# Optimization experiments

Measured on AMD Instinct MI355X. Metric: run time of the kernel, lower is better.

## Reference

```python
import jax, jax.numpy as jnp
import numpy as np

NUM_HEADS = 16

def setup_inputs() -> dict:
    key = jax.random.key(0)
    kq, kk, kv = jax.random.split(key, 3)
    B, S, D = 4, 2048, 1024
    return {
        "queries": jax.random.normal(kq, (B, S, D), dtype=jnp.float32),
        "keys": jax.random.normal(kk, (B, S, D), dtype=jnp.float32),
        "values": jax.random.normal(kv, (B, S, D), dtype=jnp.float32),
    }

def _split_heads(x):
    # [B, S, D] -> [B, H, S, Dh]
    B, S, D = x.shape
    return x.reshape(B, S, NUM_HEADS, D // NUM_HEADS).transpose(0, 2, 1, 3)

def reference(queries, keys, values):
    q = _split_heads(queries)   # [B, H, S, Dh]
    k = _split_heads(keys)
    v = _split_heads(values)
    d_k = k.shape[-1]
    scale = 1.0 / jnp.sqrt(jnp.asarray(d_k, dtype=q.dtype))
    # [B, H, S, S] score matrix (materialized, as in the original bmm path)
    scores = jnp.einsum('bhqd,bhkd->bhqk', q, k) * scale
    weights = jax.nn.softmax(scores, axis=-1)
    out = jnp.einsum('bhqk,bhkd->bhqd', weights, v)  # [B, H, S, Dh]
    B, H, S, Dh = out.shape
    return out.transpose(0, 2, 1, 3).reshape(B, S, H * Dh)
```

## Files before the change

kernel.cpp:

```cpp
#include <hip/hip_runtime.h>
#include <hip/hip_bf16.h>
#include <math.h>

#define SEQ    2048
#define NH     16
#define DH     64
#define DMODEL 1024
#define KT     64
#define NT     (SEQ/KT)
#define KH_BYTES (4 * NH * SEQ * DH * 2)

typedef __bf16 bf16x8 __attribute__((ext_vector_type(8)));
typedef float  f32x4  __attribute__((ext_vector_type(4)));
typedef float  f32x16 __attribute__((ext_vector_type(16)));
typedef unsigned u32x2 __attribute__((ext_vector_type(2)));
typedef unsigned short u16x8 __attribute__((ext_vector_type(8)));
typedef __attribute__((address_space(3))) unsigned int        lds_u32_t;
typedef __attribute__((address_space(1))) const unsigned int  g_u32_t;

__device__ __forceinline__ ushort f2bf(float f) {
    union { __hip_bfloat16 h; ushort u; } z;
    z.h = __float2bfloat16(f);
    return z.u;
}

__device__ __forceinline__ unsigned pk2(float lo, float hi) {
    unsigned r;
    asm("v_cvt_pk_bf16_f32 %0, %1, %2" : "=v"(r) : "v"(lo), "v"(hi));
    return r;
}

__device__ __forceinline__ void load16(const char* g, char* l) {
    __builtin_amdgcn_global_load_lds((g_u32_t*)g, (lds_u32_t*)l, 16, 0, 0);
}

__global__ __launch_bounds__(256)
void prep_kv(const float* __restrict__ K, const float* __restrict__ V,
             ushort* __restrict__ Kh, ushort* __restrict__ Vt) {
    int blk = blockIdx.x;
    int tid = threadIdx.x;
    if (blk < 2048) {
        int i = tid >> 6;
        int c = tid & 63;
        int g = blk * 4 + i;
        int b = g >> 11, s = g & 2047;
        int h = c >> 2, d0 = (c & 3) * 16;
        const float* kp = K + (size_t)g * DMODEL + c * 16;
        float4 f0 = ((const float4*)kp)[0];
        float4 f1 = ((const float4*)kp)[1];
        float4 f2 = ((const float4*)kp)[2];
        float4 f3 = ((const float4*)kp)[3];
        u16x8 a, bq;
        a[0]=f2bf(f0.x); a[1]=f2bf(f0.y); a[2]=f2bf(f0.z); a[3]=f2bf(f0.w);
        a[4]=f2bf(f1.x); a[5]=f2bf(f1.y); a[6]=f2bf(f1.z); a[7]=f2bf(f1.w);
        bq[0]=f2bf(f2.x); bq[1]=f2bf(f2.y); bq[2]=f2bf(f2.z); bq[3]=f2bf(f2.w);
        bq[4]=f2bf(f3.x); bq[5]=f2bf(f3.y); bq[6]=f2bf(f3.z); bq[7]=f2bf(f3.w);
        ushort* op = Kh + ((size_t)(b * NH + h) * SEQ + s) * DH + d0;
        *(u16x8*)op = a;
        *(u16x8*)(op + 8) = bq;
    } else {
        int vb = blk - 2048;
        int st = vb & 31, bh = vb >> 5;
        int b = bh >> 4, h = bh & 15;
        int s0 = st * 64;
        int s4 = tid >> 4, dg = tid & 15;
        const float* vp = V + ((size_t)(b * SEQ + s0 + s4 * 4)) * DMODEL + h * DH + dg * 4;
        float4 r0 = ((const float4*)vp)[0];
        float4 r1 = *(const float4*)(vp + DMODEL);
        float4 r2 = *(const float4*)(vp + 2 * DMODEL);
        float4 r3 = *(const float4*)(vp + 3 * DMODEL);
        ushort4 w0 = make_ushort4(f2bf(r0.x), f2bf(r1.x), f2bf(r2.x), f2bf(r3.x));
        ushort4 w1 = make_ushort4(f2bf(r0.y), f2bf(r1.y), f2bf(r2.y), f2bf(r3.y));
        ushort4 w2 = make_ushort4(f2bf(r0.z), f2bf(r1.z), f2bf(r2.z), f2bf(r3.z));
        ushort4 w3 = make_ushort4(f2bf(r0.w), f2bf(r1.w), f2bf(r2.w), f2bf(r3.w));
        size_t vbase = ((size_t)bh * DH) * SEQ + s0 + s4 * 4;
        *(ushort4*)(Vt + vbase + (size_t)(dg * 4 + 0) * SEQ) = w0;
        *(ushort4*)(Vt + vbase + (size_t)(dg * 4 + 1) * SEQ) = w1;
        *(ushort4*)(Vt + vbase + (size_t)(dg * 4 + 2) * SEQ) = w2;
        *(ushort4*)(Vt + vbase + (size_t)(dg * 4 + 3) * SEQ) = w3;
    }
}

__global__ __launch_bounds__(256, 2)
void mha_fwd32(const float* __restrict__ Q, const ushort* __restrict__ Kh,
               const ushort* __restrict__ Vt, float* __restrict__ Out) {
    int raw = blockIdx.x;
    int bid = (raw & 7) * 64 + (raw >> 3);
    int qt = bid & 7;
    int bh = bid >> 3;
    int b = bh >> 4, h = bh & 15;

    const int tid  = threadIdx.x;
    const int lane = tid & 63;
    const int w    = tid >> 6;
    const int l31  = lane & 31;
    const int lh   = lane >> 5;

    __shared__ __attribute__((aligned(16))) ushort Ks[2][KT * DH];
    __shared__ __attribute__((aligned(16))) ushort Vs[2][KT * DH];

    int o0  = tid * 16;
    int o1  = o0 + 4096;
    int so0 = o0 ^ (((o0 >> 7) & 7) << 4);
    int so1 = o1 ^ (((o1 >> 7) & 7) << 4);
    const char* khead = (const char*)Kh + (size_t)bh * (SEQ * DH * 2);
    const char* vhead = (const char*)Vt + (size_t)bh * (SEQ * DH * 2);
    const char* kg0 = khead + so0;
    const char* kg1 = khead + so1;
    const char* vg0 = vhead + (size_t)(o0 >> 7) * (SEQ * 2) + (so0 & 127);
    const char* vg1 = vhead + (size_t)(o1 >> 7) * (SEQ * 2) + (so1 & 127);

    const float QSCALE = 0.125f * 1.4426950408889634f;
    bf16x8 qf[2][4];
    #pragma unroll
    for (int q2 = 0; q2 < 2; ++q2) {
        int qrow = qt * 256 + w * 64 + q2 * 32 + l31;
        const float* qp = Q + ((size_t)b * SEQ + qrow) * DMODEL + h * DH + lh * 8;
        #pragma unroll
        for (int ks = 0; ks < 4; ++ks) {
            float4 fa = *(const float4*)(qp + ks * 16);
            float4 fb = *(const float4*)(qp + ks * 16 + 4);
            union { unsigned u[4]; bf16x8 v; } z;
            z.u[0] = pk2(fa.x * QSCALE, fa.y * QSCALE);
            z.u[1] = pk2(fa.z * QSCALE, fa.w * QSCALE);
            z.u[2] = pk2(fb.x * QSCALE, fb.y * QSCALE);
            z.u[3] = pk2(fb.z * QSCALE, fb.w * QSCALE);
            qf[q2][ks] = z.v;
        }
    }

    f32x16 oacc[2][2];
    #pragma unroll
    for (int a = 0; a < 2; ++a)
        #pragma unroll
        for (int d = 0; d < 2; ++d)
            #pragma unroll
            for (int i = 0; i < 16; ++i) oacc[a][d][i] = 0.f;
    float lacc0 = 0.f, lacc1 = 0.f;

    int swz = (l31 & 7) << 4;
    int offRd[2][4];
    #pragma unroll
    for (int x = 0; x < 2; ++x)
        #pragma unroll
        for (int ks = 0; ks < 4; ++ks)
            offRd[x][ks] = (x * 32 + l31) * 128 + ((ks * 32 + lh * 16) ^ swz);

    {
        char* kb = (char*)&Ks[0][0] + w * 1024;
        char* vb = (char*)&Vs[0][0] + w * 1024;
        load16(kg0, kb); load16(kg1, kb + 4096);
        load16(vg0, vb); load16(vg1, vb + 4096);
        kg0 += KT * DH * 2; kg1 += KT * DH * 2; vg0 += KT * 2; vg1 += KT * 2;
    }
    __syncthreads();

    int buf = 0;
    for (int kt = 0; kt < NT; ++kt) {
        if (kt + 1 < NT) {
            char* kb = (char*)&Ks[buf ^ 1][0] + w * 1024;
            char* vb = (char*)&Vs[buf ^ 1][0] + w * 1024;
            load16(kg0, kb); load16(kg1, kb + 4096);
            load16(vg0, vb); load16(vg1, vb + 4096);
            kg0 += KT * DH * 2; kg1 += KT * DH * 2; vg0 += KT * 2; vg1 += KT * 2;
        }
        const char* kbb = (const char*)&Ks[buf][0];
        const char* vbb = (const char*)&Vs[buf][0];

        f32x16 sc[2][2];
        #pragma unroll
        for (int a = 0; a < 2; ++a)
            #pragma unroll
            for (int t = 0; t < 2; ++t)
                #pragma unroll
                for (int i = 0; i < 16; ++i) sc[a][t][i] = 0.f;

        __builtin_amdgcn_s_setprio(1);
        #pragma unroll
        for (int t = 0; t < 2; ++t) {
            #pragma unroll
            for (int ks = 0; ks < 4; ++ks) {
                bf16x8 kf = *(const bf16x8*)(kbb + offRd[t][ks]);
                sc[0][t] = __builtin_amdgcn_mfma_f32_32x32x16_bf16(kf, qf[0][ks], sc[0][t], 0, 0, 0);
                sc[1][t] = __builtin_amdgcn_mfma_f32_32x32x16_bf16(kf, qf[1][ks], sc[1][t], 0, 0, 0);
            }
        }
        __builtin_amdgcn_s_setprio(0);

        bf16x8 pa[2][4];
        #pragma unroll
        for (int q2 = 0; q2 < 2; ++q2) {
            float e[2][16];
            #pragma unroll
            for (int t = 0; t < 2; ++t)
                #pragma unroll
                for (int r = 0; r < 16; ++r)
                    e[t][r] = exp2f(fminf(sc[q2][t][r], 80.f));
            float s0 = 0.f, s1 = 0.f, s2 = 0.f, s3 = 0.f;
            #pragma unroll
            for (int t = 0; t < 2; ++t)
                #pragma unroll
                for (int m = 0; m < 4; ++m) {
                    s0 += e[t][4 * m + 0]; s1 += e[t][4 * m + 1];
                    s2 += e[t][4 * m + 2]; s3 += e[t][4 * m + 3];
                }
            if (q2 == 0) lacc0 += (s0 + s1) + (s2 + s3);
            else         lacc1 += (s0 + s1) + (s2 + s3);
            #pragma unroll
            for (int t = 0; t < 2; ++t) {
                #pragma unroll
                for (int s = 0; s < 2; ++s) {
                    unsigned X  = pk2(e[t][8 * s + 0], e[t][8 * s + 1]);
                    unsigned Bw = pk2(e[t][8 * s + 2], e[t][8 * s + 3]);
                    unsigned Y  = pk2(e[t][8 * s + 4], e[t][8 * s + 5]);
                    unsigned Dw = pk2(e[t][8 * s + 6], e[t][8 * s + 7]);
                    u32x2 pq = __builtin_amdgcn_permlane32_swap(X, Y, false, false);
                    u32x2 rs = __builtin_amdgcn_permlane32_swap(Bw, Dw, false, false);
                    union { unsigned u[4]; bf16x8 v; } z;
                    z.u[0] = pq.x; z.u[1] = rs.x; z.u[2] = pq.y; z.u[3] = rs.y;
                    pa[q2][2 * t + s] = z.v;
                }
            }
        }

        __builtin_amdgcn_s_setprio(1);
        #pragma unroll
        for (int dt = 0; dt < 2; ++dt) {
            #pragma unroll
            for (int ks = 0; ks < 4; ++ks) {
                bf16x8 vf = *(const bf16x8*)(vbb + offRd[dt][ks]);
                oacc[0][dt] = __builtin_amdgcn_mfma_f32_32x32x16_bf16(pa[0][ks], vf, oacc[0][dt], 0, 0, 0);
                oacc[1][dt] = __builtin_amdgcn_mfma_f32_32x32x16_bf16(pa[1][ks], vf, oacc[1][dt], 0, 0, 0);
            }
        }
        __builtin_amdgcn_s_setprio(0);

        __syncthreads();
        buf ^= 1;
    }

    #pragma unroll
    for (int q2 = 0; q2 < 2; ++q2) {
        float la = (q2 == 0) ? lacc0 : lacc1;
        float lt = la + __shfl_xor(la, 32);
        float rl = 1.0f / lt;
        #pragma unroll
        for (int r = 0; r < 16; ++r) {
            int qp_ = (r & 3) + 8 * (r >> 2) + 4 * lh;
            float rlr = __shfl(rl, (lane & 32) | qp_);
            int qrow = qt * 256 + w * 64 + q2 * 32 + qp_;
            float* op = Out + ((size_t)b * SEQ + qrow) * DMODEL + h * DH + l31;
            op[0]  = oacc[q2][0][r] * rlr;
            op[32] = oacc[q2][1][r] * rlr;
        }
    }
}

__global__ __launch_bounds__(256)
void mha_fwd_fallback(const float* __restrict__ Q, const float* __restrict__ K,
                      const float* __restrict__ V, float* __restrict__ Out) {
    int raw = blockIdx.x;
    int bid = (raw & 7) * 256 + (raw >> 3);
    int qt = bid & 31;
    int bh = bid >> 5;
    int b  = bh >> 4;
    int h  = bh & 15;
    const int tid  = threadIdx.x;
    const int lane = tid & 63;
    const int w    = tid >> 6;
    const int l15  = lane & 15;
    const int g    = lane >> 4;
    __shared__ ushort KsS[KT * DH];
    __shared__ ushort VTS[DH * KT];
    __shared__ ushort PlS[4][16 * KT];
    char* KsB = (char*)KsS;
    char* VTB = (char*)VTS;
    char* PlB = (char*)&PlS[w][0];
    const size_t base = ((size_t)b * SEQ) * DMODEL + (size_t)h * DH;
    const float QSCALE = 0.125f * 1.4426950408889634f;
    bf16x8 qa[2];
    {
        int qrow = qt * 64 + w * 16 + l15;
        const float* qp = Q + base + (size_t)qrow * DMODEL;
        for (int ds = 0; ds < 2; ++ds) {
            float4 f0 = *(const float4*)(qp + ds * 32 + g * 8);
            float4 f1 = *(const float4*)(qp + ds * 32 + g * 8 + 4);
            union { ushort u[8]; bf16x8 v; } pk;
            pk.u[0] = f2bf(f0.x * QSCALE); pk.u[1] = f2bf(f0.y * QSCALE);
            pk.u[2] = f2bf(f0.z * QSCALE); pk.u[3] = f2bf(f0.w * QSCALE);
            pk.u[4] = f2bf(f1.x * QSCALE); pk.u[5] = f2bf(f1.y * QSCALE);
            pk.u[6] = f2bf(f1.z * QSCALE); pk.u[7] = f2bf(f1.w * QSCALE);
            qa[ds] = pk.v;
        }
    }
    f32x4 oacc[4];
    for (int i = 0; i < 4; ++i) { oacc[i][0]=0.f; oacc[i][1]=0.f; oacc[i][2]=0.f; oacc[i][3]=0.f; }
    float m_r[4], l_r[4];
    for (int r = 0; r < 4; ++r) { m_r[r] = -3.0e38f; l_r[r] = 0.f; }
    for (int kt = 0; kt < SEQ / KT; ++kt) {
        const int kbase = kt * KT;
        for (int i = 0; i < 4; ++i) {
            int pos  = i * 256 + tid;
            int krow = pos >> 4;
            int d4   = (pos & 15) * 4;
            const float* kp = K + base + (size_t)(kbase + krow) * DMODEL + d4;
            float4 f = *(const float4*)kp;
            ushort4 u = make_ushort4(f2bf(f.x), f2bf(f.y), f2bf(f.z), f2bf(f.w));
            int off = (krow * 128 + d4 * 2) ^ ((krow & 7) << 4);
            *(ushort4*)(KsB + off) = u;
        }
        {
            int kg = tid >> 4;
            int d4 = (tid & 15) * 4;
            const float* vp = V + base + (size_t)(kbase + kg * 4) * DMODEL + d4;
            float4 r0 = *(const float4*)(vp);
            float4 r1 = *(const float4*)(vp + DMODEL);
            float4 r2 = *(const float4*)(vp + 2 * DMODEL);
            float4 r3 = *(const float4*)(vp + 3 * DMODEL);
            ushort4 c0 = make_ushort4(f2bf(r0.x), f2bf(r1.x), f2bf(r2.x), f2bf(r3.x));
            ushort4 c1 = make_ushort4(f2bf(r0.y), f2bf(r1.y), f2bf(r2.y), f2bf(r3.y));
            ushort4 c2 = make_ushort4(f2bf(r0.z), f2bf(r1.z), f2bf(r2.z), f2bf(r3.z));
            ushort4 c3 = make_ushort4(f2bf(r0.w), f2bf(r1.w), f2bf(r2.w), f2bf(r3.w));
            int row, off;
            row = d4 + 0; off = (row * 128 + kg * 8) ^ ((row & 7) << 4); *(ushort4*)(VTB + off) = c0;
            row = d4 + 1; off = (row * 128 + kg * 8) ^ ((row & 7) << 4); *(ushort4*)(VTB + off) = c1;
            row = d4 + 2; off = (row * 128 + kg * 8) ^ ((row & 7) << 4); *(ushort4*)(VTB + off) = c2;
            row = d4 + 3; off = (row * 128 + kg * 8) ^ ((row & 7) << 4); *(ushort4*)(VTB + off) = c3;
        }
        __syncthreads();
        f32x4 sc[4];
        for (int sub = 0; sub < 4; ++sub) {
            f32x4 a; a[0]=0.f; a[1]=0.f; a[2]=0.f; a[3]=0.f;
            for (int ds = 0; ds < 2; ++ds) {
                int krow = sub * 16 + l15;
                int off = (krow * 128 + ds * 64 + g * 16) ^ ((krow & 7) << 4);
                bf16x8 kb = *(const bf16x8*)(KsB + off);
                a = __builtin_amdgcn_mfma_f32_16x16x32_bf16(qa[ds], kb, a, 0, 0, 0);
            }
            sc[sub] = a;
        }
        float corr[4];
        float p[4][4];
        for (int r = 0; r < 4; ++r) {
            float t = fmaxf(fmaxf(sc[0][r], sc[1][r]), fmaxf(sc[2][r], sc[3][r]));
            t = fmaxf(t, __shfl_xor(t, 1));
            t = fmaxf(t, __shfl_xor(t, 2));
            t = fmaxf(t, __shfl_xor(t, 4));
            t = fmaxf(t, __shfl_xor(t, 8));
            float mn = fmaxf(m_r[r], t);
            corr[r] = exp2f(m_r[r] - mn);
            m_r[r] = mn;
            float s = 0.f;
            for (int sub = 0; sub < 4; ++sub) {
                float e = exp2f(sc[sub][r] - mn);
                p[sub][r] = e;
                s += e;
            }
            s += __shfl_xor(s, 1);
            s += __shfl_xor(s, 2);
            s += __shfl_xor(s, 4);
            s += __shfl_xor(s, 8);
            l_r[r] = l_r[r] * corr[r] + s;
        }
        for (int dsub = 0; dsub < 4; ++dsub)
            for (int r = 0; r < 4; ++r)
                oacc[dsub][r] *= corr[r];
        for (int r = 0; r < 4; ++r) {
            int row = g * 4 + r;
            for (int sub = 0; sub < 4; ++sub) {
                int off = (row * 128 + (sub * 16 + l15) * 2) ^ ((row & 7) << 4);
                *(ushort*)(PlB + off) = f2bf(p[sub][r]);
            }
        }
        bf16x8 pa[2];
        for (int ks = 0; ks < 2; ++ks) {
            int off = (l15 * 128 + ks * 64 + g * 16) ^ ((l15 & 7) << 4);
            pa[ks] = *(const bf16x8*)(PlB + off);
        }
        for (int dsub = 0; dsub < 4; ++dsub) {
            f32x4 a = oacc[dsub];
            for (int ks = 0; ks < 2; ++ks) {
                int row = dsub * 16 + l15;
                int off = (row * 128 + ks * 64 + g * 16) ^ ((row & 7) << 4);
                bf16x8 vb = *(const bf16x8*)(VTB + off);
                a = __builtin_amdgcn_mfma_f32_16x16x32_bf16(pa[ks], vb, a, 0, 0, 0);
            }
            oacc[dsub] = a;
        }
        __syncthreads();
    }
    for (int r = 0; r < 4; ++r) {
        float rl = 1.0f / l_r[r];
        int qrow = qt * 64 + w * 16 + g * 4 + r;
        float* op = Out + ((size_t)b * SEQ + qrow) * DMODEL + (size_t)h * DH;
        for (int dsub = 0; dsub < 4; ++dsub)
            op[dsub * 16 + l15] = oacc[dsub][r] * rl;
    }
}

extern "C" void kernel_launch(void* const* d_in, const int* in_sizes, int n_in,
                              void* d_out, int out_size, void* d_ws, size_t ws_size,
                              hipStream_t stream) {
    const float* Q = (const float*)d_in[0];
    const float* K = (const float*)d_in[1];
    const float* V = (const float*)d_in[2];
    float* Out = (float*)d_out;

    if (ws_size >= (size_t)2 * KH_BYTES) {
        ushort* Kh = (ushort*)d_ws;
        ushort* Vt = (ushort*)((char*)d_ws + KH_BYTES);
        prep_kv<<<dim3(4096), dim3(256), 0, stream>>>(K, V, Kh, Vt);
        mha_fwd32<<<dim3(512), dim3(256), 0, stream>>>(Q, Kh, Vt, Out);
    } else {
        mha_fwd_fallback<<<dim3(2048), dim3(256), 0, stream>>>(Q, K, V, Out);
    }
}
```

Baseline: 243.9 us.

## Compute softmax row sums via MFMA with ones and transpose V through LDS

The softmax denominator now comes from extra MFMAs that multiply the bf16 probabilities by a ones matrix, replacing the per-element VALU adds and the cross-lane shuffles. exp2f with clamping becomes the raw v_exp_f32 builtin, the first QK MFMA takes a zero accumulator instead of zero-initialising the score registers, and the final division uses the fast reciprocal. The V transpose in the prep kernel is staged through swizzled LDS so global reads and writes are coalesced. In exchange this adds 8 MFMAs per tile, computes the row sum from bf16-rounded probabilities, and drops the overflow clamp, which could affect accuracy.

```diff
diff --git a/kernel.cpp b/kernel.cpp
--- a/kernel.cpp
+++ b/kernel.cpp
@@ -30,6 +30,14 @@
     return r;
 }
 
+__device__ __forceinline__ float fexp2(float x) {
+#if __has_builtin(__builtin_amdgcn_exp2f)
+    return __builtin_amdgcn_exp2f(x);
+#else
+    float r; asm("v_exp_f32 %0, %1\n\ts_nop 0" : "=v"(r) : "v"(x)); return r;
+#endif
+}
+
 __device__ __forceinline__ void load16(const char* g, char* l) {
     __builtin_amdgcn_global_load_lds((g_u32_t*)g, (lds_u32_t*)l, 16, 0, 0);
 }
@@ -37,6 +45,7 @@
 __global__ __launch_bounds__(256)
 void prep_kv(const float* __restrict__ K, const float* __restrict__ V,
              ushort* __restrict__ Kh, ushort* __restrict__ Vt) {
+    __shared__ __attribute__((aligned(16))) ushort T[64 * 64];
     int blk = blockIdx.x;
     int tid = threadIdx.x;
     if (blk < 2048) {
@@ -63,21 +72,42 @@
         int st = vb & 31, bh = vb >> 5;
         int b = bh >> 4, h = bh & 15;
         int s0 = st * 64;
-        int s4 = tid >> 4, dg = tid & 15;
-        const float* vp = V + ((size_t)(b * SEQ + s0 + s4 * 4)) * DMODEL + h * DH + dg * 4;
-        float4 r0 = ((const float4*)vp)[0];
-        float4 r1 = *(const float4*)(vp + DMODEL);
-        float4 r2 = *(const float4*)(vp + 2 * DMODEL);
-        float4 r3 = *(const float4*)(vp + 3 * DMODEL);
-        ushort4 w0 = make_ushort4(f2bf(r0.x), f2bf(r1.x), f2bf(r2.x), f2bf(r3.x));
-        ushort4 w1 = make_ushort4(f2bf(r0.y), f2bf(r1.y), f2bf(r2.y), f2bf(r3.y));
-        ushort4 w2 = make_ushort4(f2bf(r0.z), f2bf(r1.z), f2bf(r2.z), f2bf(r3.z));
-        ushort4 w3 = make_ushort4(f2bf(r0.w), f2bf(r1.w), f2bf(r2.w), f2bf(r3.w));
-        size_t vbase = ((size_t)bh * DH) * SEQ + s0 + s4 * 4;
-        *(ushort4*)(Vt + vbase + (size_t)(dg * 4 + 0) * SEQ) = w0;
-        *(ushort4*)(Vt + vbase + (size_t)(dg * 4 + 1) * SEQ) = w1;
-        *(ushort4*)(Vt + vbase + (size_t)(dg * 4 + 2) * SEQ) = w2;
-        *(ushort4*)(Vt + vbase + (size_t)(dg * 4 + 3) * SEQ) = w3;
+        char* TB = (char*)T;
+        {
+            int sr = tid >> 2, seg = tid & 3;
+            const float* vp = V + ((size_t)(b * SEQ + s0 + sr)) * DMODEL + h * DH + seg * 16;
+            float4 f0 = ((const float4*)vp)[0];
+            float4 f1 = ((const float4*)vp)[1];
+            float4 f2 = ((const float4*)vp)[2];
+            float4 f3 = ((const float4*)vp)[3];
+            union { unsigned u[4]; u16x8 v; } za, zb;
+            za.u[0] = pk2(f0.x, f0.y); za.u[1] = pk2(f0.z, f0.w);
+            za.u[2] = pk2(f1.x, f1.y); za.u[3] = pk2(f1.z, f1.w);
+            zb.u[0] = pk2(f2.x, f2.y); zb.u[1] = pk2(f2.z, f2.w);
+            zb.u[2] = pk2(f3.x, f3.y); zb.u[3] = pk2(f3.z, f3.w);
+            int base = sr * 128 + seg * 32;
+            int sw = (sr & 7) << 4;
+            *(u16x8*)(TB + ((base) ^ sw))      = za.v;
+            *(u16x8*)(TB + ((base + 16) ^ sw)) = zb.v;
+        }
+        __syncthreads();
+        {
+            int dr = tid >> 2, sseg = tid & 3;
+            u16x8 o0, o1;
+            #pragma unroll
+            for (int i = 0; i < 8; ++i) {
+                int s = sseg * 16 + i;
+                o0[i] = *(const ushort*)(TB + ((s * 128 + dr * 2) ^ ((s & 7) << 4)));
+            }
+            #pragma unroll
+            for (int i = 0; i < 8; ++i) {
+                int s = sseg * 16 + 8 + i;
+                o1[i] = *(const ushort*)(TB + ((s * 128 + dr * 2) ^ ((s & 7) << 4)));
+            }
+            ushort* op = Vt + ((size_t)(bh * DH + dr)) * SEQ + s0 + sseg * 16;
+            *(u16x8*)op = o0;
+            *(u16x8*)(op + 8) = o1;
+        }
     }
 }
 
@@ -129,6 +159,17 @@
         }
     }
 
+    f32x16 zro;
+    #pragma unroll
+    for (int i = 0; i < 16; ++i) zro[i] = 0.f;
+    bf16x8 onesf;
+    {
+        union { unsigned u[4]; bf16x8 v; } z;
+        z.u[0] = 0x3F803F80u; z.u[1] = 0x3F803F80u;
+        z.u[2] = 0x3F803F80u; z.u[3] = 0x3F803F80u;
+        onesf = z.v;
+    }
+
     f32x16 oacc[2][2];
     #pragma unroll
     for (int a = 0; a < 2; ++a)
@@ -136,7 +177,11 @@
         for (int d = 0; d < 2; ++d)
             #pragma unroll
             for (int i = 0; i < 16; ++i) oacc[a][d][i] = 0.f;
-    float lacc0 = 0.f, lacc1 = 0.f;
+    f32x16 lacc[2];
+    #pragma unroll
+    for (int a = 0; a < 2; ++a)
+        #pragma unroll
+        for (int i = 0; i < 16; ++i) lacc[a][i] = 0.f;
 
     int swz = (l31 & 7) << 4;
     int offRd[2][4];
@@ -168,21 +213,19 @@
         const char* vbb = (const char*)&Vs[buf][0];
 
         f32x16 sc[2][2];
-        #pragma unroll
-        for (int a = 0; a < 2; ++a)
-            #pragma unroll
-            for (int t = 0; t < 2; ++t)
-                #pragma unroll
-                for (int i = 0; i < 16; ++i) sc[a][t][i] = 0.f;
-
         __builtin_amdgcn_s_setprio(1);
         #pragma unroll
         for (int t = 0; t < 2; ++t) {
             #pragma unroll
             for (int ks = 0; ks < 4; ++ks) {
                 bf16x8 kf = *(const bf16x8*)(kbb + offRd[t][ks]);
-                sc[0][t] = __builtin_amdgcn_mfma_f32_32x32x16_bf16(kf, qf[0][ks], sc[0][t], 0, 0, 0);
-                sc[1][t] = __builtin_amdgcn_mfma_f32_32x32x16_bf16(kf, qf[1][ks], sc[1][t], 0, 0, 0);
+                if (ks == 0) {
+                    sc[0][t] = __builtin_amdgcn_mfma_f32_32x32x16_bf16(kf, qf[0][0], zro, 0, 0, 0);
+                    sc[1][t] = __builtin_amdgcn_mfma_f32_32x32x16_bf16(kf, qf[1][0], zro, 0, 0, 0);
+                } else {
+                    sc[0][t] = __builtin_amdgcn_mfma_f32_32x32x16_bf16(kf, qf[0][ks], sc[0][t], 0, 0, 0);
+                    sc[1][t] = __builtin_amdgcn_mfma_f32_32x32x16_bf16(kf, qf[1][ks], sc[1][t], 0, 0, 0);
+                }
             }
         }
         __builtin_amdgcn_s_setprio(0);
@@ -195,17 +238,7 @@
             for (int t = 0; t < 2; ++t)
                 #pragma unroll
                 for (int r = 0; r < 16; ++r)
-                    e[t][r] = exp2f(fminf(sc[q2][t][r], 80.f));
-            float s0 = 0.f, s1 = 0.f, s2 = 0.f, s3 = 0.f;
-            #pragma unroll
-            for (int t = 0; t < 2; ++t)
-                #pragma unroll
-                for (int m = 0; m < 4; ++m) {
-                    s0 += e[t][4 * m + 0]; s1 += e[t][4 * m + 1];
-                    s2 += e[t][4 * m + 2]; s3 += e[t][4 * m + 3];
-                }
-            if (q2 == 0) lacc0 += (s0 + s1) + (s2 + s3);
-            else         lacc1 += (s0 + s1) + (s2 + s3);
+                    e[t][r] = fexp2(sc[q2][t][r]);
             #pragma unroll
             for (int t = 0; t < 2; ++t) {
                 #pragma unroll
@@ -233,6 +266,11 @@
                 oacc[1][dt] = __builtin_amdgcn_mfma_f32_32x32x16_bf16(pa[1][ks], vf, oacc[1][dt], 0, 0, 0);
             }
         }
+        #pragma unroll
+        for (int ks = 0; ks < 4; ++ks) {
+            lacc[0] = __builtin_amdgcn_mfma_f32_32x32x16_bf16(pa[0][ks], onesf, lacc[0], 0, 0, 0);
+            lacc[1] = __builtin_amdgcn_mfma_f32_32x32x16_bf16(pa[1][ks], onesf, lacc[1], 0, 0, 0);
+        }
         __builtin_amdgcn_s_setprio(0);
 
         __syncthreads();
@@ -241,17 +279,14 @@
 
     #pragma unroll
     for (int q2 = 0; q2 < 2; ++q2) {
-        float la = (q2 == 0) ? lacc0 : lacc1;
-        float lt = la + __shfl_xor(la, 32);
-        float rl = 1.0f / lt;
         #pragma unroll
         for (int r = 0; r < 16; ++r) {
+            float rl = __builtin_amdgcn_rcpf(lacc[q2][r]);
             int qp_ = (r & 3) + 8 * (r >> 2) + 4 * lh;
-            float rlr = __shfl(rl, (lane & 32) | qp_);
             int qrow = qt * 256 + w * 64 + q2 * 32 + qp_;
             float* op = Out + ((size_t)b * SEQ + qrow) * DMODEL + h * DH + l31;
-            op[0]  = oacc[q2][0][r] * rlr;
-            op[32] = oacc[q2][1][r] * rlr;
+            op[0]  = oacc[q2][0][r] * rl;
+            op[32] = oacc[q2][1][r] * rl;
         }
     }
 }
@@ -271,7 +306,7 @@
     const int l15  = lane & 15;
     const int g    = lane >> 4;
     __shared__ ushort KsS[KT * DH];
-    __shared__ ushort VTS[DH * KT];
+    __shared__ ushort VTS[KT * DH];
     __shared__ ushort PlS[4][16 * KT];
     char* KsB = (char*)KsS;
     char* VTB = (char*)VTS;
```

After: 200.8 us. 1.21x faster.
